# Kernel tuning notes

Hardware: AMD Instinct MI355X
Metric: run time of the kernel (lower is better)

The kernel has to match this reference:

```python
import jax, jax.numpy as jnp
import numpy as np

B, W, C_BLK, N_EMBD, N_HEADS = 512, 128, 24, 32, 2


def setup_inputs() -> dict:
    key = jax.random.key(0)
    k1, k2, k3, k4 = jax.random.split(key, 4)
    x = jax.random.normal(k1, (B, W, C_BLK, N_EMBD), dtype=jnp.float32)
    x_end_idx = jax.random.randint(k2, (B, W), 0, C_BLK, dtype=jnp.int32)
    # nn.Linear(n_embd, 3*n_embd, bias=False): store transposed so y = x @ w
    w_attn = jax.random.normal(k3, (N_EMBD, 3 * N_EMBD), dtype=jnp.float32) * (1.0 / np.sqrt(N_EMBD))
    w_proj = jax.random.normal(k4, (N_EMBD, N_EMBD), dtype=jnp.float32) * (1.0 / np.sqrt(N_EMBD))
    return {"x": x, "x_end_idx": x_end_idx, "w_attn": w_attn, "w_proj": w_proj}


def reference(x, x_end_idx, w_attn, w_proj):
    # x: [B, W, c, C]; causal self-attention over the char axis c, per (batch, word).
    Bd, Wd, c, C = x.shape
    H = N_HEADS
    D = C // H
    qkv = x @ w_attn                               # [B, W, c, 3C]
    q, k, v = jnp.split(qkv, 3, axis=-1)
    # [B, W, H, c, D]
    q = q.reshape(Bd, Wd, c, H, D).transpose(0, 1, 3, 2, 4)
    k = k.reshape(Bd, Wd, c, H, D).transpose(0, 1, 3, 2, 4)
    v = v.reshape(Bd, Wd, c, H, D).transpose(0, 1, 3, 2, 4)
    scale = 1.0 / jnp.sqrt(jnp.asarray(D, dtype=x.dtype))
    scores = jnp.einsum('bwhqd,bwhkd->bwhqk', q, k) * scale   # [B, W, H, c, c]
    causal = jnp.tril(jnp.ones((c, c), dtype=bool))
    scores = jnp.where(causal, scores, jnp.asarray(-jnp.inf, dtype=scores.dtype))
    att = jax.nn.softmax(scores, axis=-1)
    out = jnp.einsum('bwhqk,bwhkd->bwhqd', att, v)            # [B, W, H, c, D]
    out = out.transpose(0, 1, 3, 2, 4).reshape(Bd, Wd, c, C)
    out = out @ w_proj                                        # c_proj (dropout in eval mode = identity)
    out = x + out                                             # residual
    # Vectorized last-token gather: pick out[b, w, x_end_idx[b, w], :]
    idx = x_end_idx[:, :, None, None].astype(jnp.int32)       # [B, W, 1, 1]
    samples = jnp.take_along_axis(out, jnp.broadcast_to(idx, (Bd, Wd, 1, C)), axis=2)
    return samples.squeeze(2)                                 # [B, W, C]
```

## Files before the change

kernel.cpp:

```cpp
#include <hip/hip_runtime.h>


#define CB      24
#define CC      32
#define DD      16
#define THREEC  96
#define NBW     (512 * 128)
#define WPB     4
#define XSS     34

__device__ __align__(16) float4 g_M4[2][8][CC];
__device__ __align__(16) float4 g_P4[2][8][CC];

__global__ void precompute_mp(const float* __restrict__ w_attn,
                              const float* __restrict__ w_proj)
{
    const int idx = blockIdx.x * 256 + threadIdx.x;
    const int h = idx >> 8, e4 = (idx >> 5) & 7, c = idx & 31;
    float m[4], p[4];
    #pragma unroll
    for (int k = 0; k < 4; ++k) {
        const int e = 4 * e4 + k;
        float mm = 0.f, pp = 0.f;
        #pragma unroll
        for (int d = 0; d < DD; ++d) {
            const int i = DD * h + d;
            mm = fmaf(w_attn[e * THREEC + i],          w_attn[c * THREEC + CC + i], mm);
            pp = fmaf(w_attn[e * THREEC + 2 * CC + i], w_proj[i * CC + c],          pp);
        }
        m[k] = 0.25f * mm;
        p[k] = pp;
    }
    g_M4[h][e4][c] = make_float4(m[0], m[1], m[2], m[3]);
    g_P4[h][e4][c] = make_float4(p[0], p[1], p[2], p[3]);
}

struct __align__(16) WaveSmem {
    float xs[CB][XSS];
    float rks[2][CC];
    float ps[2][CC];
    float ys[2][CC];
};

__device__ __forceinline__ void wave_fence() {
    __asm__ volatile("s_waitcnt lgkmcnt(0)" ::: "memory");
}

__global__ __launch_bounds__(256, 8) void char_attn_kernel(
    const float* __restrict__ x,
    const int*   __restrict__ xend,
    float*       __restrict__ out)
{
    __shared__ WaveSmem sm[WPB];

    const int tid  = threadIdx.x;
    const int lane = tid & 63;
    const int wave = tid >> 6;
    WaveSmem& S = sm[wave];

    const int i32  = lane & 31;
    const int half = lane >> 5;

    const int sbid = __builtin_amdgcn_readfirstlane(blockIdx.x * WPB + wave);
    const int sq   = __builtin_amdgcn_readfirstlane(xend[sbid]);
    const int L    = sq + 1;

    const float* __restrict__ xb = x + (size_t)sbid * (CB * CC);
    const float* __restrict__ xq = xb + sq * CC;

    {
        const float2* xb2 = (const float2*)xb;
        const int n2 = L * (CC / 2);
        for (int t = lane; t < n2; t += 64) {
            float2 v = xb2[t];
            const int r = t >> 4, c = (t & 15) * 2;
            *(float2*)&S.xs[r][c] = v;
        }
    }

    {
        float a0 = 0.f, a1 = 0.f, a2 = 0.f, a3 = 0.f;
        #pragma unroll
        for (int e4 = 0; e4 < 8; ++e4) {
            const float4 mv = g_M4[half][e4][i32];
            const float4 xv = *(const float4*)(xq + e4 * 4);
            a0 = fmaf(mv.x, xv.x, a0);
            a1 = fmaf(mv.y, xv.y, a1);
            a2 = fmaf(mv.z, xv.z, a2);
            a3 = fmaf(mv.w, xv.w, a3);
        }
        S.rks[half][i32] = (a0 + a1) + (a2 + a3);
    }
    wave_fence();

    {
        float sc = -INFINITY;
        if (i32 <= sq) {
            const float4* rk4 = (const float4*)&S.rks[half][0];
            float a0 = 0.f, a1 = 0.f, a2 = 0.f, a3 = 0.f;
            #pragma unroll
            for (int e4 = 0; e4 < 8; ++e4) {
                const float4 rv = rk4[e4];
                const float2 x0 = *(const float2*)&S.xs[i32][e4 * 4];
                const float2 x1 = *(const float2*)&S.xs[i32][e4 * 4 + 2];
                a0 = fmaf(rv.x, x0.x, a0);
                a1 = fmaf(rv.y, x0.y, a1);
                a2 = fmaf(rv.z, x1.x, a2);
                a3 = fmaf(rv.w, x1.y, a3);
            }
            sc = (a0 + a1) + (a2 + a3);
        }
        float m = sc;
        #pragma unroll
        for (int off = 16; off >= 1; off >>= 1)
            m = fmaxf(m, __shfl_xor(m, off));
        const float e = (i32 <= sq) ? __expf(sc - m) : 0.f;
        float sum = e;
        #pragma unroll
        for (int off = 16; off >= 1; off >>= 1)
            sum += __shfl_xor(sum, off);
        S.ps[half][i32] = __fdividef(e, sum);
    }
    wave_fence();

    {
        float a0 = 0.f, a1 = 0.f;
        int j = 0;
        for (; j + 1 < L; j += 2) {
            const float2 p2 = *(const float2*)&S.ps[half][j];
            a0 = fmaf(p2.x, S.xs[j][i32],     a0);
            a1 = fmaf(p2.y, S.xs[j + 1][i32], a1);
        }
        if (j < L)
            a0 = fmaf(S.ps[half][j], S.xs[j][i32], a0);
        S.ys[half][i32] = a0 + a1;
    }
    wave_fence();

    {
        const float4* y4 = (const float4*)&S.ys[half][0];
        float a0 = 0.f, a1 = 0.f, a2 = 0.f, a3 = 0.f;
        #pragma unroll
        for (int e4 = 0; e4 < 8; ++e4) {
            const float4 pv = g_P4[half][e4][i32];
            const float4 yv = y4[e4];
            a0 = fmaf(pv.x, yv.x, a0);
            a1 = fmaf(pv.y, yv.y, a1);
            a2 = fmaf(pv.z, yv.z, a2);
            a3 = fmaf(pv.w, yv.w, a3);
        }
        float t = (a0 + a1) + (a2 + a3);
        t += __shfl_xor(t, 32);
        if (lane < CC)
            out[(size_t)sbid * CC + i32] = t + S.xs[sq][i32];
    }
}

extern "C" void kernel_launch(void* const* d_in, const int* in_sizes, int n_in,
                              void* d_out, int out_size, void* d_ws, size_t ws_size,
                              hipStream_t stream) {
    const float* x      = (const float*)d_in[0];
    const int*   xend   = (const int*)d_in[1];
    const float* w_attn = (const float*)d_in[2];
    const float* w_proj = (const float*)d_in[3];
    float* out = (float*)d_out;

    precompute_mp<<<dim3(2), dim3(256), 0, stream>>>(w_attn, w_proj);
    char_attn_kernel<<<dim3(NBW / WPB), dim3(WPB * 64), 0, stream>>>(
        x, xend, out);
}
```

Baseline: 294.6 us.

## Drop softmax max-subtraction, widen x loads, and double waves per block

Raises waves per block from 4 to 8 and widens the x staging loads from float2 to float4. The query-row vector is preloaded into registers, and the softmax max-reduction is removed. Normalisation is folded into a single reciprocal multiply after the weighted sum. Skipping the max subtraction saves five shuffles and a divide per lane, but it risks exp overflow on large scores, and the rows with i32 > sq now read uninitialised shared memory (masked afterwards).

```diff
diff --git a/kernel.cpp b/kernel.cpp
--- a/kernel.cpp
+++ b/kernel.cpp
@@ -6,7 +6,8 @@
 #define DD      16
 #define THREEC  96
 #define NBW     (512 * 128)
-#define WPB     4
+#define WPB     8
+#define NBLK    (NBW / WPB)
 #define XSS     34
 
 __device__ __align__(16) float4 g_M4[2][8][CC];
@@ -46,7 +47,7 @@
     __asm__ volatile("s_waitcnt lgkmcnt(0)" ::: "memory");
 }
 
-__global__ __launch_bounds__(256, 8) void char_attn_kernel(
+__global__ __launch_bounds__(512, 8) void char_attn_kernel(
     const float* __restrict__ x,
     const int*   __restrict__ xend,
     float*       __restrict__ out)
@@ -68,13 +69,18 @@
     const float* __restrict__ xb = x + (size_t)sbid * (CB * CC);
     const float* __restrict__ xq = xb + sq * CC;
 
+    float4 xqv[8];
+    #pragma unroll
+    for (int e = 0; e < 8; ++e) xqv[e] = *(const float4*)(xq + 4 * e);
+
     {
-        const float2* xb2 = (const float2*)xb;
-        const int n2 = L * (CC / 2);
-        for (int t = lane; t < n2; t += 64) {
-            float2 v = xb2[t];
-            const int r = t >> 4, c = (t & 15) * 2;
-            *(float2*)&S.xs[r][c] = v;
+        const float4* xb4 = (const float4*)xb;
+        const int n4 = L * (CC / 4);
+        for (int t = lane; t < n4; t += 64) {
+            const float4 v = xb4[t];
+            const int r = t >> 3, c = (t & 7) * 4;
+            *(float2*)&S.xs[r][c]     = make_float2(v.x, v.y);
+            *(float2*)&S.xs[r][c + 2] = make_float2(v.z, v.w);
         }
     }
 
@@ -83,43 +89,36 @@
         #pragma unroll
         for (int e4 = 0; e4 < 8; ++e4) {
             const float4 mv = g_M4[half][e4][i32];
-            const float4 xv = *(const float4*)(xq + e4 * 4);
-            a0 = fmaf(mv.x, xv.x, a0);
-            a1 = fmaf(mv.y, xv.y, a1);
-            a2 = fmaf(mv.z, xv.z, a2);
-            a3 = fmaf(mv.w, xv.w, a3);
+            a0 = fmaf(mv.x, xqv[e4].x, a0);
+            a1 = fmaf(mv.y, xqv[e4].y, a1);
+            a2 = fmaf(mv.z, xqv[e4].z, a2);
+            a3 = fmaf(mv.w, xqv[e4].w, a3);
         }
         S.rks[half][i32] = (a0 + a1) + (a2 + a3);
     }
     wave_fence();
 
+    float rsum;
     {
-        float sc = -INFINITY;
-        if (i32 <= sq) {
-            const float4* rk4 = (const float4*)&S.rks[half][0];
-            float a0 = 0.f, a1 = 0.f, a2 = 0.f, a3 = 0.f;
-            #pragma unroll
-            for (int e4 = 0; e4 < 8; ++e4) {
-                const float4 rv = rk4[e4];
-                const float2 x0 = *(const float2*)&S.xs[i32][e4 * 4];
-                const float2 x1 = *(const float2*)&S.xs[i32][e4 * 4 + 2];
-                a0 = fmaf(rv.x, x0.x, a0);
-                a1 = fmaf(rv.y, x0.y, a1);
-                a2 = fmaf(rv.z, x1.x, a2);
-                a3 = fmaf(rv.w, x1.y, a3);
-            }
-            sc = (a0 + a1) + (a2 + a3);
+        const float4* rk4 = (const float4*)&S.rks[half][0];
+        float a0 = 0.f, a1 = 0.f, a2 = 0.f, a3 = 0.f;
+        #pragma unroll
+        for (int e4 = 0; e4 < 8; ++e4) {
+            const float4 rv = rk4[e4];
+            const float2 x0 = *(const float2*)&S.xs[i32][e4 * 4];
+            const float2 x1 = *(const float2*)&S.xs[i32][e4 * 4 + 2];
+            a0 = fmaf(rv.x, x0.x, a0);
+            a1 = fmaf(rv.y, x0.y, a1);
+            a2 = fmaf(rv.z, x1.x, a2);
+            a3 = fmaf(rv.w, x1.y, a3);
         }
-        float m = sc;
-        #pragma unroll
-        for (int off = 16; off >= 1; off >>= 1)
-            m = fmaxf(m, __shfl_xor(m, off));
-        const float e = (i32 <= sq) ? __expf(sc - m) : 0.f;
+        const float e = (i32 <= sq) ? __expf((a0 + a1) + (a2 + a3)) : 0.f;
+        S.ps[half][i32] = e;
         float sum = e;
         #pragma unroll
         for (int off = 16; off >= 1; off >>= 1)
             sum += __shfl_xor(sum, off);
-        S.ps[half][i32] = __fdividef(e, sum);
+        rsum = __fdividef(1.f, sum);
     }
     wave_fence();
 
@@ -133,7 +132,7 @@
         }
         if (j < L)
             a0 = fmaf(S.ps[half][j], S.xs[j][i32], a0);
-        S.ys[half][i32] = a0 + a1;
+        S.ys[half][i32] = (a0 + a1) * rsum;
     }
     wave_fence();
 
@@ -166,6 +165,6 @@
     float* out = (float*)d_out;
 
     precompute_mp<<<dim3(2), dim3(256), 0, stream>>>(w_attn, w_proj);
-    char_attn_kernel<<<dim3(NBW / WPB), dim3(WPB * 64), 0, stream>>>(
+    char_attn_kernel<<<dim3(NBLK), dim3(WPB * 64), 0, stream>>>(
         x, xend, out);
 }
```

Measured after the change: 289.7 us. Within noise of the previous version (-1.7%).
